# Optimization experiments

Measured on AMD Instinct MI355X. Metric: run time of the kernel, lower is better.

The kernel has to match this reference:

```python
import jax, jax.numpy as jnp
import numpy as np

NUM_HEAD = 8
HIDDEN = 128
NLAYERS = 6
NUM_FREQ = HIDDEN // 2


def make_pe_table(w):
    # relative positions in [-(w-1), w-1] -> raw angle table (the torch code
    # indexes `pe` BEFORE sin/cos are applied, so the table holds raw angles)
    rel = jnp.arange(w)[None, :] - jnp.arange(w)[:, None]          # [w, w]
    idx = (rel + (w - 1)).reshape(-1)
    rel_s2l = jnp.arange(2 * w - 1, dtype=jnp.float32) - (w - 1)   # [2w-1]
    freqs = jnp.arange(NUM_FREQ * 2)
    dim = jnp.power(jnp.float32(10000.0), (2 * (freqs // 2) / HIDDEN).astype(jnp.float32))
    pe = rel_s2l[:, None] / dim[None, :]                           # [2w-1, 128]
    return pe[idx].reshape(w, w, HIDDEN)


def layer_norm(x, g, b, eps=1e-5):
    mu = x.mean(-1, keepdims=True)
    var = ((x - mu) ** 2).mean(-1, keepdims=True)
    return (x - mu) / jnp.sqrt(var + eps) * g + b


def attention(Wi, bi, Wo, bo, query, key, pe_table, is_cross):
    w, h, c = query.shape
    hd = c // NUM_HEAD
    if is_cross:
        q = query @ Wi[:c].T + bi[:c]
        kv = key @ Wi[c:].T + bi[c:]
        k, v = jnp.split(kv, 2, axis=-1)
    else:
        q, k, v = jnp.split(query @ Wi.T + bi, 3, axis=-1)
    q = q.reshape(w, h, NUM_HEAD, hd)
    k = k.reshape(w, h, NUM_HEAD, hd)
    v = v.reshape(w, h, NUM_HEAD, hd)
    attn = jnp.einsum('whnc,vhnc->hnwv', q, k)                      # [h, nh, w, w]
    # relative PE terms: project pe_table with the q and k input projections
    rpe = pe_table @ Wi[:2 * c].T + bi[:2 * c]                       # [w, w, 2c]
    q_rpe, k_rpe = jnp.split(rpe, 2, axis=-1)
    q_rpe = q_rpe.reshape(w, w, NUM_HEAD, hd)
    k_rpe = k_rpe.reshape(w, w, NUM_HEAD, hd)
    attn = attn + jnp.einsum('wnec,wvec->newv', q, k_rpe) + jnp.einsum('vnec,wvec->newv', k, q_rpe)
    attn = attn / (hd ** 0.5)
    score = attn.sum(axis=1)                                         # [h, w, w]
    p = jax.nn.softmax(attn, axis=-1)
    out = jnp.einsum('hnwv,vhnc->whnc', p, v).reshape(w, h, c)
    return out @ Wo.T + bo, score


# mirror torch.utils.checkpoint on every attention call
_self_attn = jax.checkpoint(lambda Wi, bi, Wo, bo, x, pe: attention(Wi, bi, Wo, bo, x, x, pe, False))
_cross_attn = jax.checkpoint(lambda Wi, bi, Wo, bo, q, k, pe: attention(Wi, bi, Wo, bo, q, k, pe, True))


def forward(x_l, x_r, feat_w, feat_b, self_Wi, self_bi, self_Wo, self_bo,
            cross_Wi, cross_bi, cross_Wo, cross_bo, ln_g, ln_b):
    b, c, h, w = x_l.shape
    # FeatEx modeled as learned 1x1 conv c -> HIDDEN
    xl = jnp.einsum('bchw,dc->bdhw', x_l, feat_w) + feat_b[None, :, None, None]
    xr = jnp.einsum('bchw,dc->bdhw', x_r, feat_w) + feat_b[None, :, None, None]
    pe_table = make_pe_table(w)
    # (b,c,h,w) -> (w, h*b, c): width is the sequence axis
    xl = xl.transpose(3, 2, 0, 1).reshape(w, h * b, HIDDEN)
    xr = xr.transpose(3, 2, 0, 1).reshape(w, h * b, HIDDEN)
    cross_score = None
    for i in range(NLAYERS):
        xl = layer_norm(xl, ln_g, ln_b)
        o, _ = _self_attn(self_Wi[i], self_bi[i], self_Wo[i], self_bo[i], xl, pe_table)
        xl = xl + o
        xr = layer_norm(xr, ln_g, ln_b)
        o, _ = _self_attn(self_Wi[i], self_bi[i], self_Wo[i], self_bo[i], xr, pe_table)
        xr = xr + o
        xl = layer_norm(xl, ln_g, ln_b)
        xr = layer_norm(xr, ln_g, ln_b)
        o, cross_score = _cross_attn(cross_Wi[i], cross_bi[i], cross_Wo[i], cross_bo[i], xr, xl, pe_table)
        xl = xl + o
    u = jnp.arange(w, dtype=jnp.float32)
    corresp = (jax.nn.softmax(cross_score, axis=-1) * u[None, None, :]).sum(-1)  # [h*b, w]
    return u[None, None, :] - corresp.reshape(b, h, w)


def setup_inputs() -> dict:
    key = jax.random.key(0)
    ks = jax.random.split(key, 8)
    b, cin, h, w = 2, 128, 64, 224
    s = 0.02
    return {
        'x_l': jax.random.normal(ks[0], (b, cin, h, w), jnp.float32),
        'x_r': jax.random.normal(ks[1], (b, cin, h, w), jnp.float32),
        'feat_w': jax.random.normal(ks[2], (HIDDEN, cin), jnp.float32) * s,
        'feat_b': jnp.zeros((HIDDEN,), jnp.float32),
        'self_Wi': jax.random.normal(ks[3], (NLAYERS, 3 * HIDDEN, HIDDEN), jnp.float32) * s,
        'self_bi': jnp.zeros((NLAYERS, 3 * HIDDEN), jnp.float32),
        'self_Wo': jax.random.normal(ks[4], (NLAYERS, HIDDEN, HIDDEN), jnp.float32) * s,
        'self_bo': jnp.zeros((NLAYERS, HIDDEN), jnp.float32),
        'cross_Wi': jax.random.normal(ks[5], (NLAYERS, 3 * HIDDEN, HIDDEN), jnp.float32) * s,
        'cross_bi': jnp.zeros((NLAYERS, 3 * HIDDEN), jnp.float32),
        'cross_Wo': jax.random.normal(ks[6], (NLAYERS, HIDDEN, HIDDEN), jnp.float32) * s,
        'cross_bo': jnp.zeros((NLAYERS, HIDDEN), jnp.float32),
        'ln_g': jnp.ones((HIDDEN,), jnp.float32),
        'ln_b': jnp.zeros((HIDDEN,), jnp.float32),
    }


def reference(x_l, x_r, feat_w, feat_b, self_Wi, self_bi, self_Wo, self_bo,
              cross_Wi, cross_bi, cross_Wo, cross_bo, ln_g, ln_b):
    return forward(x_l, x_r, feat_w, feat_b, self_Wi, self_bi, self_Wo, self_bo,
                   cross_Wi, cross_bi, cross_Wo, cross_bo, ln_g, ln_b)
```

## Files before the change

### kernel.cpp

```cpp
#include <hip/hip_runtime.h>

typedef unsigned short u16;
typedef unsigned int u32;

#define W_ 224
#define H_ 128
#define C_ 128
#define NH 8
#define HD 16
#define ROWS_ (W_ * H_)
#define PREP_STRIDE 4128
#define KSTR 40
#define VSTR 232
#define TROWS 32

typedef __bf16 bf16x8 __attribute__((ext_vector_type(8)));
typedef float f32x4 __attribute__((ext_vector_type(4)));

__device__ __forceinline__ u16 f2bf(float f) {
  u32 u = __float_as_uint(f);
  return (u16)((u + 0x7FFFu + ((u >> 16) & 1u)) >> 16);
}
__device__ __forceinline__ u32 cvtpk(float lo, float hi) {
  u32 r;
  asm("v_cvt_pk_bf16_f32 %0, %1, %2" : "=v"(r) : "v"(lo), "v"(hi));
  return r;
}

__global__ __launch_bounds__(256) void prep_kernel(
    const float* __restrict__ self_Wi, const float* __restrict__ self_bi,
    const float* __restrict__ cross_Wi, const float* __restrict__ cross_bi,
    float* __restrict__ prep) {
  __shared__ float Wq[16][132];
  __shared__ float Wk[16][132];
  __shared__ float u[128];
  __shared__ float Aq[16], Ak[16], bq[16], bk[16];
  const int s = blockIdx.x, e = blockIdx.y, l = s >> 1;
  const float* Wi = (s & 1) ? cross_Wi + (size_t)l * 384 * 128 : self_Wi + (size_t)l * 384 * 128;
  const float* bi = (s & 1) ? cross_bi + l * 384 : self_bi + l * 384;
  const int tid = threadIdx.x;
  if (tid < 128) {
    float ex = (float)(tid & ~1) * (1.f / 128.f);
    u[tid] = expf(-ex * logf(10000.f));
  }
  if (tid >= 128 && tid < 144) { int r = tid - 128; bq[r] = bi[e * 16 + r]; }
  if (tid >= 160 && tid < 176) { int r = tid - 160; bk[r] = bi[128 + e * 16 + r]; }
  for (int t = tid; t < 2048; t += 256) {
    int r = t >> 7, f = t & 127;
    Wq[r][f] = Wi[(size_t)(e * 16 + r) * 128 + f];
    Wk[r][f] = Wi[(size_t)(128 + e * 16 + r) * 128 + f];
  }
  __syncthreads();
  {
    const int grp = tid >> 3;
    const int lg = tid & 7;
    const float* row = (grp < 16) ? Wq[grp] : Wk[grp - 16];
    float a = 0.f;
#pragma unroll
    for (int i = 0; i < 16; ++i) a += row[lg * 16 + i] * u[lg * 16 + i];
    a += __shfl_xor(a, 1);
    a += __shfl_xor(a, 2);
    a += __shfl_xor(a, 4);
    if (lg == 0) {
      if (grp < 16) Aq[grp] = a;
      else          Ak[grp - 16] = a;
    }
  }
  __syncthreads();
  float* out = prep + (size_t)s * PREP_STRIDE;
  for (int t = tid; t < 512; t += 256) {
    int v = t >> 7, f = t & 127;
    float acc = 0.f;
#pragma unroll
    for (int c = 0; c < 16; ++c) {
      if (v == 0)      acc += Wq[c][f] * Ak[c];
      else if (v == 1) acc += Wq[c][f] * bk[c];
      else if (v == 2) acc += Wk[c][f] * Aq[c];
      else             acc += Wk[c][f] * bq[c];
    }
    out[v * 1024 + e * 128 + f] = acc * 0.25f;
  }
  if (tid < 4) {
    int v = tid;
    float acc = 0.f;
#pragma unroll
    for (int c = 0; c < 16; ++c) {
      if (v == 0)      acc += bq[c] * Ak[c];
      else if (v == 1) acc += bq[c] * bk[c];
      else if (v == 2) acc += bk[c] * Aq[c];
      else             acc += bk[c] * bq[c];
    }
    out[4096 + v * 8 + e] = acc * 0.25f;
  }
}

__global__ __launch_bounds__(256) void tab_kernel(
    float* __restrict__ x, const float* __restrict__ g,
    const float* __restrict__ b, const float* __restrict__ wq,
    const float* __restrict__ cq, float* __restrict__ outA, float* __restrict__ outB,
    const float* __restrict__ wk, const float* __restrict__ ck,
    float* __restrict__ outG, float* __restrict__ outD,
    u16* __restrict__ xb, int mode) {
  __shared__ float ys[TROWS][132];
  __shared__ float ws[32][132];
  const int tid = threadIdx.x;
  for (int t = tid; t < 2048; t += 256) ws[t >> 7][t & 127] = wq[t];
  for (int t = tid; t < 2048; t += 256) ws[16 + (t >> 7)][t & 127] = wk[t];
  const int wv = tid >> 6, lane = tid & 63;
  const int base = blockIdx.x * TROWS;
  {
    float2 gg = ((const float2*)g)[lane];
    float2 bb = ((const float2*)b)[lane];
    for (int t = 0; t < TROWS / 4; ++t) {
      const int r = wv * (TROWS / 4) + t;
      float2* xp = (float2*)(x + (size_t)(base + r) * 128);
      float2 v = xp[lane];
      float s1 = v.x + v.y, s2 = v.x * v.x + v.y * v.y;
#pragma unroll
      for (int k = 1; k < 64; k <<= 1) {
        s1 += __shfl_xor(s1, k);
        s2 += __shfl_xor(s2, k);
      }
      float mean = s1 * (1.f / 128.f);
      float var = s2 * (1.f / 128.f) - mean * mean;
      float rstd = rsqrtf(var + 1e-5f);
      float y0 = (v.x - mean) * rstd * gg.x + bb.x;
      float y1 = (v.y - mean) * rstd * gg.y + bb.y;
      xp[lane] = make_float2(y0, y1);
      ((u32*)xb)[(size_t)(base + r) * 64 + lane] = cvtpk(y0, y1);
      ys[r][2 * lane] = y0;
      ys[r][2 * lane + 1] = y1;
    }
  }
  __syncthreads();
  const int c = tid & 31;
  const int rg = (tid >> 5) * 4;
  const int side = c >> 4, oo = c & 15;
  const float* wrow = ws[c];
  const int val = oo >> 3, e = oo & 7;
  const float cadd = side ? ck[val * 8 + e] : cq[val * 8 + e];
  float* dst = side ? (val ? outD : outG) : (val ? outB : outA);
#pragma unroll
  for (int rr = 0; rr < 4; ++rr) {
    const int p = base + rg + rr;
    const int half = (p >= ROWS_) ? 1 : 0;
    const int ploc = p - half * ROWS_;
    const bool active = (mode == 0) || (half ? (side == 0) : (side == 1));
    if (active) {
      const float* yr = ys[rg + rr];
      float a0 = 0.f, a1 = 0.f, a2 = 0.f, a3 = 0.f;
#pragma unroll 4
      for (int f = 0; f < 128; f += 4) {
        a0 += yr[f] * wrow[f];
        a1 += yr[f + 1] * wrow[f + 1];
        a2 += yr[f + 2] * wrow[f + 2];
        a3 += yr[f + 3] * wrow[f + 3];
      }
      float acc = (a0 + a1) + (a2 + a3);
      int i = ploc >> 7, blow = ploc & 127;
      int b_out = (mode == 0) ? half * 128 + blow : blow;
      dst[((size_t)(b_out * 8 + e)) * 224 + i] = acc + cadd;
    }
  }
}

__global__ __launch_bounds__(256) void gemm_plain(
    const u16* __restrict__ A, const u16* __restrict__ B,
    const float* __restrict__ bias, int mode, float* __restrict__ fout) {
  __shared__ u16 As[64 * 136];
  __shared__ u16 Bs[64 * 136];
  const int tid = threadIdx.x;
  const int M0 = blockIdx.x * 64, N0 = blockIdx.y * 64;
  const uint4* Ag = (const uint4*)(A + (size_t)M0 * 128);
  const uint4* Bg = (const uint4*)(B + (size_t)N0 * 128);
  for (int t = tid; t < 1024; t += 256) {
    int row = t >> 4, cc = t & 15;
    *(uint4*)&As[row * 136 + cc * 8] = Ag[row * 16 + cc];
  }
  for (int t = tid; t < 1024; t += 256) {
    int row = t >> 4, cc = t & 15;
    *(uint4*)&Bs[row * 136 + cc * 8] = Bg[row * 16 + cc];
  }
  __syncthreads();
  const int wave = tid >> 6, lane = tid & 63;
  const int wm = (wave >> 1) * 32, wn = (wave & 1) * 32;
  const int lr = lane & 15, kq = (lane >> 4) * 8;
  f32x4 acc[2][2] = {};
#pragma unroll
  for (int ks = 0; ks < 4; ++ks) {
    int ko = ks * 32 + kq;
    bf16x8 a0 = *(const bf16x8*)&As[(wm + lr) * 136 + ko];
    bf16x8 a1 = *(const bf16x8*)&As[(wm + 16 + lr) * 136 + ko];
    bf16x8 b0 = *(const bf16x8*)&Bs[(wn + lr) * 136 + ko];
    bf16x8 b1 = *(const bf16x8*)&Bs[(wn + 16 + lr) * 136 + ko];
    acc[0][0] = __builtin_amdgcn_mfma_f32_16x16x32_bf16(a0, b0, acc[0][0], 0, 0, 0);
    acc[0][1] = __builtin_amdgcn_mfma_f32_16x16x32_bf16(a0, b1, acc[0][1], 0, 0, 0);
    acc[1][0] = __builtin_amdgcn_mfma_f32_16x16x32_bf16(a1, b0, acc[1][0], 0, 0, 0);
    acc[1][1] = __builtin_amdgcn_mfma_f32_16x16x32_bf16(a1, b1, acc[1][1], 0, 0, 0);
  }
  const int colq = lane & 15, rowq = (lane >> 4) * 4;
#pragma unroll
  for (int tm = 0; tm < 2; ++tm)
#pragma unroll
    for (int tn = 0; tn < 2; ++tn) {
#pragma unroll
      for (int r = 0; r < 4; ++r) {
        int row = M0 + wm + tm * 16 + rowq + r;
        int col = N0 + wn + tn * 16 + colq;
        float v = acc[tm][tn][r] + bias[col];
        if (mode == 4) fout[(size_t)row * 128 + col] += v;
        else           fout[(size_t)row * 128 + col] = v;
      }
    }
}

__global__ __launch_bounds__(256) void gemm_qkv_self(
    const u16* __restrict__ X, const u16* __restrict__ Bw,
    const float* __restrict__ bias, u16* __restrict__ o0, u16* __restrict__ o1,
    u16* __restrict__ o2) {
  __shared__ u16 As[64 * 136];
  __shared__ u16 Bs[128 * 136];
  const int tid = threadIdx.x;
  const int M0 = blockIdx.x * 64, N0 = blockIdx.y * 128;
  {
    const uint4* Bg = (const uint4*)(Bw + (size_t)N0 * 128);
    for (int t = tid; t < 2048; t += 256) {
      int row = t >> 4, cc = t & 15;
      *(uint4*)&Bs[row * 136 + cc * 8] = Bg[row * 16 + cc];
    }
  }
  {
    const uint4* Ag = (const uint4*)(X + (size_t)M0 * 128);
    for (int t = tid; t < 1024; t += 256) {
      int row = t >> 4, cc = t & 15;
      *(uint4*)&As[row * 136 + cc * 8] = Ag[row * 16 + cc];
    }
  }
  __syncthreads();
  const int wave = tid >> 6, lane = tid & 63;
  const int wm = (wave >> 1) * 32, wn = (wave & 1) * 64;
  const int lr = lane & 15, kq = (lane >> 4) * 8;
  f32x4 acc[2][4] = {};
#pragma unroll
  for (int ks = 0; ks < 4; ++ks) {
    int ko = ks * 32 + kq;
    bf16x8 a0 = *(const bf16x8*)&As[(wm + lr) * 136 + ko];
    bf16x8 a1 = *(const bf16x8*)&As[(wm + 16 + lr) * 136 + ko];
#pragma unroll
    for (int tn = 0; tn < 4; ++tn) {
      bf16x8 b0 = *(const bf16x8*)&Bs[(wn + tn * 16 + lr) * 136 + ko];
      acc[0][tn] = __builtin_amdgcn_mfma_f32_16x16x32_bf16(a0, b0, acc[0][tn], 0, 0, 0);
      acc[1][tn] = __builtin_amdgcn_mfma_f32_16x16x32_bf16(a1, b0, acc[1][tn], 0, 0, 0);
    }
  }
  const int colq = lane & 15, rowq = (lane >> 4) * 4;
#pragma unroll
  for (int tm = 0; tm < 2; ++tm)
#pragma unroll
    for (int tn = 0; tn < 4; ++tn) {
#pragma unroll
      for (int r = 0; r < 4; ++r) {
        int row = M0 + wm + tm * 16 + rowq + r;
        int col = N0 + wn + tn * 16 + colq;
        float v = acc[tm][tn][r] + bias[col];
        int part = col >> 7;
        int cc = col & 127;
        int e = cc >> 4, c = cc & 15;
        int rloc = row, badd = 0;
        if (row >= ROWS_) { rloc = row - ROWS_; badd = 128; }
        int b = (rloc & 127) + badd, pos = rloc >> 7;
        size_t off = ((size_t)(b * NH + e) * W_ + pos) * HD + c;
        if (part == 0)      o0[off] = f2bf(v * 0.25f);
        else if (part == 1) o1[off] = f2bf(v);
        else                o2[off] = f2bf(v);
      }
    }
}

__global__ __launch_bounds__(256) void gemm_qkv_cross(
    const u16* __restrict__ Xl, const u16* __restrict__ Xr,
    const u16* __restrict__ cWi, const float* __restrict__ cbi,
    u16* __restrict__ QB, u16* __restrict__ KB, u16* __restrict__ VB) {
  __shared__ u16 As[64 * 136];
  __shared__ u16 Bs[128 * 136];
  const int tid = threadIdx.x;
  const int M0 = blockIdx.x * 64;
  const int y = blockIdx.y;
  const u16* X = (y == 0) ? Xr : Xl;
  const u16* Bw = cWi + (size_t)y * 128 * 128;
  const float* bias = cbi + y * 128;
  {
    const uint4* Bg = (const uint4*)Bw;
    for (int t = tid; t < 2048; t += 256) {
      int row = t >> 4, cc = t & 15;
      *(uint4*)&Bs[row * 136 + cc * 8] = Bg[row * 16 + cc];
    }
  }
  {
    const uint4* Ag = (const uint4*)(X + (size_t)M0 * 128);
    for (int t = tid; t < 1024; t += 256) {
      int row = t >> 4, cc = t & 15;
      *(uint4*)&As[row * 136 + cc * 8] = Ag[row * 16 + cc];
    }
  }
  __syncthreads();
  const int wave = tid >> 6, lane = tid & 63;
  const int wm = (wave >> 1) * 32, wn = (wave & 1) * 64;
  const int lr = lane & 15, kq = (lane >> 4) * 8;
  f32x4 acc[2][4] = {};
#pragma unroll
  for (int ks = 0; ks < 4; ++ks) {
    int ko = ks * 32 + kq;
    bf16x8 a0 = *(const bf16x8*)&As[(wm + lr) * 136 + ko];
    bf16x8 a1 = *(const bf16x8*)&As[(wm + 16 + lr) * 136 + ko];
#pragma unroll
    for (int tn = 0; tn < 4; ++tn) {
      bf16x8 b0 = *(const bf16x8*)&Bs[(wn + tn * 16 + lr) * 136 + ko];
      acc[0][tn] = __builtin_amdgcn_mfma_f32_16x16x32_bf16(a0, b0, acc[0][tn], 0, 0, 0);
      acc[1][tn] = __builtin_amdgcn_mfma_f32_16x16x32_bf16(a1, b0, acc[1][tn], 0, 0, 0);
    }
  }
  u16* outp = (y == 0) ? QB : ((y == 1) ? KB : VB);
  const float scale = (y == 0) ? 0.25f : 1.f;
  const int colq = lane & 15, rowq = (lane >> 4) * 4;
#pragma unroll
  for (int tm = 0; tm < 2; ++tm)
#pragma unroll
    for (int tn = 0; tn < 4; ++tn) {
#pragma unroll
      for (int r = 0; r < 4; ++r) {
        int row = M0 + wm + tm * 16 + rowq + r;
        int col = wn + tn * 16 + colq;
        float v = (acc[tm][tn][r] + bias[col]) * scale;
        int e = col >> 4, c = col & 15;
        int b = row & 127, pos = row >> 7;
        outp[((size_t)(b * NH + e) * W_ + pos) * HD + c] = f2bf(v);
      }
    }
}

__global__ __launch_bounds__(448) void attn_kernel(
    const u16* __restrict__ qb, const u16* __restrict__ kb,
    const u16* __restrict__ vb, const float* __restrict__ ALPHA,
    const float* __restrict__ BETA, const float* __restrict__ GAMMA,
    const float* __restrict__ DELTA, u16* __restrict__ obuf) {
  __shared__ u16 Ksh[224 * KSTR];
  __shared__ u16 Qsh[224 * KSTR];
  __shared__ u16 Vt[16 * VSTR];
  __shared__ u16 Pbuf[7][16 * KSTR];
  const int e = blockIdx.x, b = blockIdx.y;
  const size_t hb = (size_t)(b * NH + e);
  const int tid = threadIdx.x;
  const u32 ONE = 0x3F80u;

  if (tid < 224) {
    const int j = tid;
    const uint4* src = (const uint4*)(kb + (hb * W_ + j) * HD);
    uint4 a = src[0], b2 = src[1];
    *(uint4*)&Ksh[j * KSTR] = a;
    *(uint4*)&Ksh[j * KSTR + 8] = b2;
    float G = GAMMA[hb * 224 + j];
    float D = DELTA[hb * 224 + j];
    float jf = (float)j;
    float P = G * jf + D;
    u16 Phi = f2bf(P);
    float Plo = P - __uint_as_float((u32)Phi << 16);
    u32* ex = (u32*)&Ksh[j * KSTR + 16];
    ex[0] = (u32)f2bf(G) | ((u32)Phi << 16);
    ex[1] = (u32)f2bf(Plo) | ((u32)f2bf(jf) << 16);
    ex[2] = ONE | (ONE << 16);
#pragma unroll
    for (int z = 3; z < 12; ++z) ex[z] = 0;
    const uint4* vsrc = (const uint4*)(vb + (hb * W_ + j) * HD);
    uint4 va = vsrc[0], vb4 = vsrc[1];
    u32 w[8] = {va.x, va.y, va.z, va.w, vb4.x, vb4.y, vb4.z, vb4.w};
#pragma unroll
    for (int c = 0; c < 16; ++c)
      Vt[c * VSTR + j] = (c & 1) ? (u16)(w[c >> 1] >> 16) : (u16)(w[c >> 1] & 0xFFFF);
  } else {
    const int i = tid - 224;
    const uint4* src = (const uint4*)(qb + (hb * W_ + i) * HD);
    uint4 a = src[0], b2 = src[1];
    *(uint4*)&Qsh[i * KSTR] = a;
    *(uint4*)&Qsh[i * KSTR + 8] = b2;
    float al = ALPHA[hb * 224 + i];
    float be = BETA[hb * 224 + i];
    float ifl = (float)i;
    float Q = be - al * ifl;
    u16 Qhi = f2bf(Q);
    float Qlo = Q - __uint_as_float((u32)Qhi << 16);
    u32* ex = (u32*)&Qsh[i * KSTR + 16];
    ex[0] = (u32)f2bf(-ifl) | (ONE << 16);
    ex[1] = ONE | ((u32)f2bf(al) << 16);
    ex[2] = (u32)Qhi | ((u32)f2bf(Qlo) << 16);
#pragma unroll
    for (int z = 3; z < 12; ++z) ex[z] = 0;
  }
  __syncthreads();

  const int wid = tid >> 6, lane = tid & 63;
  const int g = lane >> 4, li = lane & 15;
  u16* pb = &Pbuf[wid][0];
  const int obase = (b & 128) ? ROWS_ : 0;
  const int blow = b & 127;

  for (int qt = wid * 2; qt < wid * 2 + 2; ++qt) {
    const int i0 = qt * 16;
    const bf16x8 Bq = *(const bf16x8*)&Qsh[(i0 + li) * KSTR + g * 8];
    f32x4 C[7][2];
#pragma unroll
    for (int js = 0; js < 7; ++js) {
      const bf16x8 A0 = *(const bf16x8*)&Ksh[(js * 32 + li) * KSTR + g * 8];
      const bf16x8 A1 = *(const bf16x8*)&Ksh[(js * 32 + 16 + li) * KSTR + g * 8];
      const f32x4 Z = {0.f, 0.f, 0.f, 0.f};
      C[js][0] = __builtin_amdgcn_mfma_f32_16x16x32_bf16(A0, Bq, Z, 0, 0, 0);
      C[js][1] = __builtin_amdgcn_mfma_f32_16x16x32_bf16(A1, Bq, Z, 0, 0, 0);
    }
    float m = -1e30f;
#pragma unroll
    for (int js = 0; js < 7; ++js)
#pragma unroll
      for (int h = 0; h < 2; ++h)
        m = fmaxf(m, fmaxf(fmaxf(C[js][h][0], C[js][h][1]), fmaxf(C[js][h][2], C[js][h][3])));
    m = fmaxf(m, __shfl_xor(m, 16));
    m = fmaxf(m, __shfl_xor(m, 32));
    f32x4 O = {0.f, 0.f, 0.f, 0.f};
    float lsum = 0.f;
#pragma unroll
    for (int js = 0; js < 7; ++js) {
      float p0 = __expf(C[js][0][0] - m), p1 = __expf(C[js][0][1] - m);
      float p2 = __expf(C[js][0][2] - m), p3 = __expf(C[js][0][3] - m);
      float p4 = __expf(C[js][1][0] - m), p5 = __expf(C[js][1][1] - m);
      float p6 = __expf(C[js][1][2] - m), p7 = __expf(C[js][1][3] - m);
      lsum += ((p0 + p1) + (p2 + p3)) + ((p4 + p5) + (p6 + p7));
      u16* pr = pb + li * KSTR + g * 4;
      *(uint2*)pr = make_uint2(cvtpk(p0, p1), cvtpk(p2, p3));
      *(uint2*)(pr + 16) = make_uint2(cvtpk(p4, p5), cvtpk(p6, p7));
      const bf16x8 Ap = *(const bf16x8*)&Pbuf[wid][li * KSTR + g * 8];
      const bf16x8 Bv = *(const bf16x8*)&Vt[li * VSTR + js * 32 + g * 8];
      O = __builtin_amdgcn_mfma_f32_16x16x32_bf16(Ap, Bv, O, 0, 0, 0);
    }
    lsum += __shfl_xor(lsum, 16);
    lsum += __shfl_xor(lsum, 32);
#pragma unroll
    for (int r = 0; r < 4; ++r) {
      const float lr = __shfl(lsum, g * 4 + r);
      const int irow = i0 + g * 4 + r;
      obuf[((size_t)(obase + irow * 128 + blow)) * C_ + e * HD + li] = f2bf(O[r] * (1.f / lr));
    }
  }
}

__global__ __launch_bounds__(256) void transpose_kernel(const float* __restrict__ x_l,
                                                        const float* __restrict__ x_r,
                                                        u16* __restrict__ xT) {
  __shared__ float tile[128][57];
  const int wt = blockIdx.x * 56, hi = blockIdx.y;
  const int img = blockIdx.z >> 1, bi = blockIdx.z & 1;
  const float* x = img ? x_r : x_l;
  const int wave = threadIdx.x >> 6, lane = threadIdx.x & 63;
  for (int c = wave; c < 128; c += 4) {
    if (lane < 56)
      tile[c][lane] = x[(((size_t)bi * 128 + c) * 64 + hi) * 224 + wt + lane];
  }
  __syncthreads();
  u32* dst = (u32*)xT;
  for (int w = wave; w < 56; w += 4) {
    int p = img * ROWS_ + (wt + w) * 128 + hi * 2 + bi;
    float a = tile[lane * 2][w], b2 = tile[lane * 2 + 1][w];
    dst[(size_t)p * 64 + lane] = (u32)f2bf(a) | ((u32)f2bf(b2) << 16);
  }
}

__global__ __launch_bounds__(448) void corresp_kernel(
    const u16* __restrict__ qb, const u16* __restrict__ kb,
    const float* __restrict__ ALPHA, const float* __restrict__ BETA,
    const float* __restrict__ GAMMA, const float* __restrict__ DELTA,
    float* __restrict__ out) {
  __shared__ u16 Ksh[224 * 136];
  __shared__ float Gs[224], Ds[224];
  const int b = blockIdx.x, tid = threadIdx.x;
  if (tid < 224) {
    const int j = tid;
#pragma unroll
    for (int e = 0; e < 8; ++e) {
      const uint4* src = (const uint4*)(kb + ((size_t)(b * 8 + e) * 224 + j) * 16);
      *(uint4*)&Ksh[j * 136 + e * 16] = src[0];
      *(uint4*)&Ksh[j * 136 + e * 16 + 8] = src[1];
    }
    float gs = 0.f, ds = 0.f;
#pragma unroll
    for (int e = 0; e < 8; ++e) {
      gs += GAMMA[((size_t)(b * 8 + e)) * 224 + j];
      ds += DELTA[((size_t)(b * 8 + e)) * 224 + j];
    }
    Gs[j] = gs;
    Ds[j] = ds;
  }
  __syncthreads();
  const int wid = tid >> 6, lane = tid & 63;
  const int g = lane >> 4, li = lane & 15;
  const int i = blockIdx.y * 112 + wid * 16 + li;
  bf16x8 Bq[4];
#pragma unroll
  for (int ks = 0; ks < 4; ++ks) {
    const int e2 = ks * 2 + (g >> 1), c0 = (g & 1) * 8;
    Bq[ks] = *(const bf16x8*)&qb[((size_t)(b * 8 + e2) * 224 + i) * 16 + c0];
  }
  f32x4 C[14];
#pragma unroll
  for (int js = 0; js < 14; ++js) {
    f32x4 acc = {0.f, 0.f, 0.f, 0.f};
#pragma unroll
    for (int ks = 0; ks < 4; ++ks) {
      const bf16x8 A = *(const bf16x8*)&Ksh[(js * 16 + li) * 136 + ks * 32 + g * 8];
      acc = __builtin_amdgcn_mfma_f32_16x16x32_bf16(A, Bq[ks], acc, 0, 0, 0);
    }
    C[js] = acc;
  }
  float ai = 0.f, bi_ = 0.f;
#pragma unroll
  for (int e = 0; e < 8; ++e) {
    ai += ALPHA[((size_t)(b * 8 + e)) * 224 + i];
    bi_ += BETA[((size_t)(b * 8 + e)) * 224 + i];
  }
  const float ifl = (float)i;
  float m = -1e30f;
#pragma unroll
  for (int js = 0; js < 14; ++js) {
#pragma unroll
    for (int r = 0; r < 4; ++r) {
      const int j = js * 16 + g * 4 + r;
      float s = C[js][r] + ((float)j - ifl) * (ai + Gs[j]) + bi_ + Ds[j];
      C[js][r] = s;
      m = fmaxf(m, s);
    }
  }
  m = fmaxf(m, __shfl_xor(m, 16));
  m = fmaxf(m, __shfl_xor(m, 32));
  float l = 0.f, wj = 0.f;
#pragma unroll
  for (int js = 0; js < 14; ++js) {
#pragma unroll
    for (int r = 0; r < 4; ++r) {
      const float p = __expf(C[js][r] - m);
      l += p;
      wj += p * (float)(js * 16 + g * 4 + r);
    }
  }
  l += __shfl_xor(l, 16);
  l += __shfl_xor(l, 32);
  wj += __shfl_xor(wj, 16);
  wj += __shfl_xor(wj, 32);
  if (g == 0) out[(size_t)b * 224 + i] = ifl - wj / fmaxf(l, 1e-30f);
}

#define OFF_FEAT 0
#define OFF_SWI 16384
#define OFF_SWO 311296
#define OFF_CWI 409600
#define OFF_CWO 704512
#define N_WALL 802816
__global__ __launch_bounds__(256) void cvt_all_kernel(
    const float* __restrict__ feat_w, const float* __restrict__ self_Wi,
    const float* __restrict__ self_Wo, const float* __restrict__ cross_Wi,
    const float* __restrict__ cross_Wo, u16* __restrict__ dst) {
  int idx = blockIdx.x * 256 + threadIdx.x;
  if (idx >= N_WALL) return;
  float v;
  if (idx < OFF_SWI)       v = feat_w[idx];
  else if (idx < OFF_SWO)  v = self_Wi[idx - OFF_SWI];
  else if (idx < OFF_CWI)  v = self_Wo[idx - OFF_SWO];
  else if (idx < OFF_CWO)  v = cross_Wi[idx - OFF_CWI];
  else                     v = cross_Wo[idx - OFF_CWO];
  dst[idx] = f2bf(v);
}

extern "C" void kernel_launch(void* const* d_in, const int* in_sizes, int n_in,
                              void* d_out, int out_size, void* d_ws, size_t ws_size,
                              hipStream_t stream) {
  (void)in_sizes; (void)n_in; (void)out_size; (void)ws_size;
  const float* x_l = (const float*)d_in[0];
  const float* x_r = (const float*)d_in[1];
  const float* feat_w = (const float*)d_in[2];
  const float* feat_b = (const float*)d_in[3];
  const float* self_Wi = (const float*)d_in[4];
  const float* self_bi = (const float*)d_in[5];
  const float* self_Wo = (const float*)d_in[6];
  const float* self_bo = (const float*)d_in[7];
  const float* cross_Wi = (const float*)d_in[8];
  const float* cross_bi = (const float*)d_in[9];
  const float* cross_Wo = (const float*)d_in[10];
  const float* cross_bo = (const float*)d_in[11];
  const float* ln_g = (const float*)d_in[12];
  const float* ln_b = (const float*)d_in[13];

  char* ws = (char*)d_ws;
  size_t off = 0;
  auto alloc = [&](size_t bytes) {
    char* p = ws + off;
    off += (bytes + 255) & ~(size_t)255;
    return p;
  };
  float* XA = (float*)alloc((size_t)2 * ROWS_ * C_ * 4);
  u16* QB = (u16*)alloc((size_t)256 * NH * W_ * HD * 2);
  u16* KB = (u16*)alloc((size_t)256 * NH * W_ * HD * 2);
  u16* VB = (u16*)alloc((size_t)256 * NH * W_ * HD * 2);
  u16* OB = (u16*)alloc((size_t)2 * ROWS_ * C_ * 2);
  u16* WALL = (u16*)alloc((size_t)N_WALL * 2);
  float* PREP = (float*)alloc((size_t)12 * PREP_STRIDE * 4);
  float* ALPHA = (float*)alloc((size_t)256 * NH * W_ * 4);
  float* BETA = (float*)alloc((size_t)256 * NH * W_ * 4);
  float* GAMMA = (float*)alloc((size_t)256 * NH * W_ * 4);
  float* DELTA = (float*)alloc((size_t)256 * NH * W_ * 4);
  u16* XB = OB;

  cvt_all_kernel<<<3136, 256, 0, stream>>>(feat_w, self_Wi, self_Wo, cross_Wi, cross_Wo, WALL);
  prep_kernel<<<dim3(12, 8), 256, 0, stream>>>(self_Wi, self_bi, cross_Wi, cross_bi, PREP);

  transpose_kernel<<<dim3(4, 64, 4), 256, 0, stream>>>(x_l, x_r, QB);
  gemm_plain<<<dim3(896, 2), 256, 0, stream>>>(QB, WALL + OFF_FEAT, feat_b, 5, XA);

  for (int l = 0; l < 6; ++l) {
    const u16* sWi = WALL + OFF_SWI + (size_t)l * 384 * 128;
    const u16* sWo = WALL + OFF_SWO + (size_t)l * 128 * 128;
    const u16* cWi = WALL + OFF_CWI + (size_t)l * 384 * 128;
    const u16* cWo = WALL + OFF_CWO + (size_t)l * 128 * 128;
    const float* sbi = self_bi + l * 384;
    const float* sbo = self_bo + l * 128;
    const float* cbi = cross_bi + l * 384;
    const float* cbo = cross_bo + l * 128;
    const float* ps = PREP + (size_t)(l * 2) * PREP_STRIDE;
    const float* pc = PREP + (size_t)(l * 2 + 1) * PREP_STRIDE;

    tab_kernel<<<1792, 256, 0, stream>>>(XA, ln_g, ln_b, ps, ps + 4096, ALPHA, BETA,
                                         ps + 2048, ps + 4112, GAMMA, DELTA, XB, 0);
    gemm_qkv_self<<<dim3(896, 3), 256, 0, stream>>>(XB, sWi, sbi, QB, KB, VB);
    attn_kernel<<<dim3(8, 256), 448, 0, stream>>>(QB, KB, VB, ALPHA, BETA, GAMMA, DELTA, OB);
    gemm_plain<<<dim3(896, 2), 256, 0, stream>>>(OB, sWo, sbo, 4, XA);

    tab_kernel<<<1792, 256, 0, stream>>>(XA, ln_g, ln_b, pc, pc + 4096, ALPHA, BETA,
                                         pc + 2048, pc + 4112, GAMMA, DELTA, XB, 1);
    gemm_qkv_cross<<<dim3(448, 3), 256, 0, stream>>>(XB, XB + (size_t)ROWS_ * C_, cWi, cbi,
                                                     QB, KB, VB);
    if (l < 5) {
      attn_kernel<<<dim3(8, 128), 448, 0, stream>>>(QB, KB, VB, ALPHA, BETA, GAMMA, DELTA, OB);
      gemm_plain<<<dim3(448, 2), 256, 0, stream>>>(OB, cWo, cbo, 4, XA);
    }
  }
  corresp_kernel<<<dim3(128, 2), 448, 0, stream>>>(QB, KB, ALPHA, BETA, GAMMA, DELTA,
                                                   (float*)d_out);
}
```

Baseline: 1.263 ms.

## Keep softmax probabilities in registers, use exp2, enlarge QKV GEMM tiles

```diff
diff --git a/kernel.cpp b/kernel.cpp
--- a/kernel.cpp
+++ b/kernel.cpp
@@ -26,6 +26,14 @@
   asm("v_cvt_pk_bf16_f32 %0, %1, %2" : "=v"(r) : "v"(lo), "v"(hi));
   return r;
 }
+__device__ __forceinline__ float bflo(u32 u) { return __uint_as_float(u << 16); }
+__device__ __forceinline__ float bfhi(u32 u) { return __uint_as_float(u & 0xFFFF0000u); }
+
+#if __has_builtin(__builtin_amdgcn_exp2f)
+#define EX2(x) __builtin_amdgcn_exp2f(x)
+#else
+#define EX2(x) __expf((x) * 0.6931471805599453f)
+#endif
 
 __global__ __launch_bounds__(256) void prep_kernel(
     const float* __restrict__ self_Wi, const float* __restrict__ self_bi,
@@ -102,7 +110,7 @@
     float* __restrict__ outG, float* __restrict__ outD,
     u16* __restrict__ xb, int mode) {
   __shared__ float ys[TROWS][132];
-  __shared__ float ws[32][132];
+  __shared__ float ws[32][133];
   const int tid = threadIdx.x;
   for (int t = tid; t < 2048; t += 256) ws[t >> 7][t & 127] = wq[t];
   for (int t = tid; t < 2048; t += 256) ws[16 + (t >> 7)][t & 127] = wk[t];
@@ -214,50 +222,45 @@
     }
 }
 
-__global__ __launch_bounds__(256) void gemm_qkv_self(
+__global__ __launch_bounds__(512) void gemm_qkv_self(
     const u16* __restrict__ X, const u16* __restrict__ Bw,
     const float* __restrict__ bias, u16* __restrict__ o0, u16* __restrict__ o1,
     u16* __restrict__ o2) {
-  __shared__ u16 As[64 * 136];
+  __shared__ u16 As[128 * 136];
   __shared__ u16 Bs[128 * 136];
   const int tid = threadIdx.x;
-  const int M0 = blockIdx.x * 64, N0 = blockIdx.y * 128;
+  const int M0 = blockIdx.x * 128, N0 = blockIdx.y * 128;
   {
     const uint4* Bg = (const uint4*)(Bw + (size_t)N0 * 128);
-    for (int t = tid; t < 2048; t += 256) {
-      int row = t >> 4, cc = t & 15;
-      *(uint4*)&Bs[row * 136 + cc * 8] = Bg[row * 16 + cc];
-    }
-  }
-  {
     const uint4* Ag = (const uint4*)(X + (size_t)M0 * 128);
-    for (int t = tid; t < 1024; t += 256) {
+    for (int t = tid; t < 2048; t += 512) {
       int row = t >> 4, cc = t & 15;
       *(uint4*)&As[row * 136 + cc * 8] = Ag[row * 16 + cc];
+      *(uint4*)&Bs[row * 136 + cc * 8] = Bg[row * 16 + cc];
     }
   }
   __syncthreads();
   const int wave = tid >> 6, lane = tid & 63;
-  const int wm = (wave >> 1) * 32, wn = (wave & 1) * 64;
+  const int wm = (wave >> 2) * 64, wn = (wave & 3) * 32;
   const int lr = lane & 15, kq = (lane >> 4) * 8;
-  f32x4 acc[2][4] = {};
+  f32x4 acc[4][2] = {};
 #pragma unroll
   for (int ks = 0; ks < 4; ++ks) {
     int ko = ks * 32 + kq;
-    bf16x8 a0 = *(const bf16x8*)&As[(wm + lr) * 136 + ko];
-    bf16x8 a1 = *(const bf16x8*)&As[(wm + 16 + lr) * 136 + ko];
-#pragma unroll
-    for (int tn = 0; tn < 4; ++tn) {
-      bf16x8 b0 = *(const bf16x8*)&Bs[(wn + tn * 16 + lr) * 136 + ko];
-      acc[0][tn] = __builtin_amdgcn_mfma_f32_16x16x32_bf16(a0, b0, acc[0][tn], 0, 0, 0);
-      acc[1][tn] = __builtin_amdgcn_mfma_f32_16x16x32_bf16(a1, b0, acc[1][tn], 0, 0, 0);
+    bf16x8 b0 = *(const bf16x8*)&Bs[(wn + lr) * 136 + ko];
+    bf16x8 b1 = *(const bf16x8*)&Bs[(wn + 16 + lr) * 136 + ko];
+#pragma unroll
+    for (int tm = 0; tm < 4; ++tm) {
+      bf16x8 a0 = *(const bf16x8*)&As[(wm + tm * 16 + lr) * 136 + ko];
+      acc[tm][0] = __builtin_amdgcn_mfma_f32_16x16x32_bf16(a0, b0, acc[tm][0], 0, 0, 0);
+      acc[tm][1] = __builtin_amdgcn_mfma_f32_16x16x32_bf16(a0, b1, acc[tm][1], 0, 0, 0);
     }
   }
   const int colq = lane & 15, rowq = (lane >> 4) * 4;
 #pragma unroll
-  for (int tm = 0; tm < 2; ++tm)
-#pragma unroll
-    for (int tn = 0; tn < 4; ++tn) {
+  for (int tm = 0; tm < 4; ++tm)
+#pragma unroll
+    for (int tn = 0; tn < 2; ++tn) {
 #pragma unroll
       for (int r = 0; r < 4; ++r) {
         int row = M0 + wm + tm * 16 + rowq + r;
@@ -277,56 +280,51 @@
     }
 }
 
-__global__ __launch_bounds__(256) void gemm_qkv_cross(
+__global__ __launch_bounds__(512) void gemm_qkv_cross(
     const u16* __restrict__ Xl, const u16* __restrict__ Xr,
     const u16* __restrict__ cWi, const float* __restrict__ cbi,
     u16* __restrict__ QB, u16* __restrict__ KB, u16* __restrict__ VB) {
-  __shared__ u16 As[64 * 136];
+  __shared__ u16 As[128 * 136];
   __shared__ u16 Bs[128 * 136];
   const int tid = threadIdx.x;
-  const int M0 = blockIdx.x * 64;
+  const int M0 = blockIdx.x * 128;
   const int y = blockIdx.y;
   const u16* X = (y == 0) ? Xr : Xl;
   const u16* Bw = cWi + (size_t)y * 128 * 128;
   const float* bias = cbi + y * 128;
   {
     const uint4* Bg = (const uint4*)Bw;
-    for (int t = tid; t < 2048; t += 256) {
-      int row = t >> 4, cc = t & 15;
-      *(uint4*)&Bs[row * 136 + cc * 8] = Bg[row * 16 + cc];
-    }
-  }
-  {
     const uint4* Ag = (const uint4*)(X + (size_t)M0 * 128);
-    for (int t = tid; t < 1024; t += 256) {
+    for (int t = tid; t < 2048; t += 512) {
       int row = t >> 4, cc = t & 15;
       *(uint4*)&As[row * 136 + cc * 8] = Ag[row * 16 + cc];
+      *(uint4*)&Bs[row * 136 + cc * 8] = Bg[row * 16 + cc];
     }
   }
   __syncthreads();
   const int wave = tid >> 6, lane = tid & 63;
-  const int wm = (wave >> 1) * 32, wn = (wave & 1) * 64;
+  const int wm = (wave >> 2) * 64, wn = (wave & 3) * 32;
   const int lr = lane & 15, kq = (lane >> 4) * 8;
-  f32x4 acc[2][4] = {};
+  f32x4 acc[4][2] = {};
 #pragma unroll
   for (int ks = 0; ks < 4; ++ks) {
     int ko = ks * 32 + kq;
-    bf16x8 a0 = *(const bf16x8*)&As[(wm + lr) * 136 + ko];
-    bf16x8 a1 = *(const bf16x8*)&As[(wm + 16 + lr) * 136 + ko];
-#pragma unroll
-    for (int tn = 0; tn < 4; ++tn) {
-      bf16x8 b0 = *(const bf16x8*)&Bs[(wn + tn * 16 + lr) * 136 + ko];
-      acc[0][tn] = __builtin_amdgcn_mfma_f32_16x16x32_bf16(a0, b0, acc[0][tn], 0, 0, 0);
-      acc[1][tn] = __builtin_amdgcn_mfma_f32_16x16x32_bf16(a1, b0, acc[1][tn], 0, 0, 0);
+    bf16x8 b0 = *(const bf16x8*)&Bs[(wn + lr) * 136 + ko];
+    bf16x8 b1 = *(const bf16x8*)&Bs[(wn + 16 + lr) * 136 + ko];
+#pragma unroll
+    for (int tm = 0; tm < 4; ++tm) {
+      bf16x8 a0 = *(const bf16x8*)&As[(wm + tm * 16 + lr) * 136 + ko];
+      acc[tm][0] = __builtin_amdgcn_mfma_f32_16x16x32_bf16(a0, b0, acc[tm][0], 0, 0, 0);
+      acc[tm][1] = __builtin_amdgcn_mfma_f32_16x16x32_bf16(a0, b1, acc[tm][1], 0, 0, 0);
     }
   }
   u16* outp = (y == 0) ? QB : ((y == 1) ? KB : VB);
   const float scale = (y == 0) ? 0.25f : 1.f;
   const int colq = lane & 15, rowq = (lane >> 4) * 4;
 #pragma unroll
-  for (int tm = 0; tm < 2; ++tm)
-#pragma unroll
-    for (int tn = 0; tn < 4; ++tn) {
+  for (int tm = 0; tm < 4; ++tm)
+#pragma unroll
+    for (int tn = 0; tn < 2; ++tn) {
 #pragma unroll
       for (int r = 0; r < 4; ++r) {
         int row = M0 + wm + tm * 16 + rowq + r;
@@ -347,11 +345,11 @@
   __shared__ u16 Ksh[224 * KSTR];
   __shared__ u16 Qsh[224 * KSTR];
   __shared__ u16 Vt[16 * VSTR];
-  __shared__ u16 Pbuf[7][16 * KSTR];
   const int e = blockIdx.x, b = blockIdx.y;
   const size_t hb = (size_t)(b * NH + e);
   const int tid = threadIdx.x;
   const u32 ONE = 0x3F80u;
+  const float LOG2E = 1.4426950408889634f;
 
   if (tid < 224) {
     const int j = tid;
@@ -362,11 +360,11 @@
     float G = GAMMA[hb * 224 + j];
     float D = DELTA[hb * 224 + j];
     float jf = (float)j;
-    float P = G * jf + D;
+    float P = (G * jf + D) * LOG2E;
     u16 Phi = f2bf(P);
     float Plo = P - __uint_as_float((u32)Phi << 16);
     u32* ex = (u32*)&Ksh[j * KSTR + 16];
-    ex[0] = (u32)f2bf(G) | ((u32)Phi << 16);
+    ex[0] = (u32)f2bf(G * LOG2E) | ((u32)Phi << 16);
     ex[1] = (u32)f2bf(Plo) | ((u32)f2bf(jf) << 16);
     ex[2] = ONE | (ONE << 16);
 #pragma unroll
@@ -374,24 +372,30 @@
     const uint4* vsrc = (const uint4*)(vb + (hb * W_ + j) * HD);
     uint4 va = vsrc[0], vb4 = vsrc[1];
     u32 w[8] = {va.x, va.y, va.z, va.w, vb4.x, vb4.y, vb4.z, vb4.w};
+    const int jl = j & 31;
+    const int qcol = (j & ~31) | (((jl >> 2) & 3) << 3) | ((jl >> 4) << 2) | (jl & 3);
 #pragma unroll
     for (int c = 0; c < 16; ++c)
-      Vt[c * VSTR + j] = (c & 1) ? (u16)(w[c >> 1] >> 16) : (u16)(w[c >> 1] & 0xFFFF);
+      Vt[c * VSTR + qcol] = (c & 1) ? (u16)(w[c >> 1] >> 16) : (u16)(w[c >> 1] & 0xFFFF);
   } else {
     const int i = tid - 224;
     const uint4* src = (const uint4*)(qb + (hb * W_ + i) * HD);
     uint4 a = src[0], b2 = src[1];
-    *(uint4*)&Qsh[i * KSTR] = a;
-    *(uint4*)&Qsh[i * KSTR + 8] = b2;
+    u32 qa[8] = {a.x, a.y, a.z, a.w, b2.x, b2.y, b2.z, b2.w};
+#pragma unroll
+    for (int t = 0; t < 8; ++t)
+      qa[t] = cvtpk(bflo(qa[t]) * LOG2E, bfhi(qa[t]) * LOG2E);
+    *(uint4*)&Qsh[i * KSTR] = make_uint4(qa[0], qa[1], qa[2], qa[3]);
+    *(uint4*)&Qsh[i * KSTR + 8] = make_uint4(qa[4], qa[5], qa[6], qa[7]);
     float al = ALPHA[hb * 224 + i];
     float be = BETA[hb * 224 + i];
     float ifl = (float)i;
-    float Q = be - al * ifl;
+    float Q = (be - al * ifl) * LOG2E;
     u16 Qhi = f2bf(Q);
     float Qlo = Q - __uint_as_float((u32)Qhi << 16);
     u32* ex = (u32*)&Qsh[i * KSTR + 16];
     ex[0] = (u32)f2bf(-ifl) | (ONE << 16);
-    ex[1] = ONE | ((u32)f2bf(al) << 16);
+    ex[1] = ONE | ((u32)f2bf(al * LOG2E) << 16);
     ex[2] = (u32)Qhi | ((u32)f2bf(Qlo) << 16);
 #pragma unroll
     for (int z = 3; z < 12; ++z) ex[z] = 0;
@@ -400,7 +404,6 @@
 
   const int wid = tid >> 6, lane = tid & 63;
   const int g = lane >> 4, li = lane & 15;
-  u16* pb = &Pbuf[wid][0];
   const int obase = (b & 128) ? ROWS_ : 0;
   const int blow = b & 127;
 
@@ -428,15 +431,13 @@
     float lsum = 0.f;
 #pragma unroll
     for (int js = 0; js < 7; ++js) {
-      float p0 = __expf(C[js][0][0] - m), p1 = __expf(C[js][0][1] - m);
-      float p2 = __expf(C[js][0][2] - m), p3 = __expf(C[js][0][3] - m);
-      float p4 = __expf(C[js][1][0] - m), p5 = __expf(C[js][1][1] - m);
-      float p6 = __expf(C[js][1][2] - m), p7 = __expf(C[js][1][3] - m);
+      float p0 = EX2(C[js][0][0] - m), p1 = EX2(C[js][0][1] - m);
+      float p2 = EX2(C[js][0][2] - m), p3 = EX2(C[js][0][3] - m);
+      float p4 = EX2(C[js][1][0] - m), p5 = EX2(C[js][1][1] - m);
+      float p6 = EX2(C[js][1][2] - m), p7 = EX2(C[js][1][3] - m);
       lsum += ((p0 + p1) + (p2 + p3)) + ((p4 + p5) + (p6 + p7));
-      u16* pr = pb + li * KSTR + g * 4;
-      *(uint2*)pr = make_uint2(cvtpk(p0, p1), cvtpk(p2, p3));
-      *(uint2*)(pr + 16) = make_uint2(cvtpk(p4, p5), cvtpk(p6, p7));
-      const bf16x8 Ap = *(const bf16x8*)&Pbuf[wid][li * KSTR + g * 8];
+      uint4 pu = make_uint4(cvtpk(p0, p1), cvtpk(p2, p3), cvtpk(p4, p5), cvtpk(p6, p7));
+      const bf16x8 Ap = __builtin_bit_cast(bf16x8, pu);
       const bf16x8 Bv = *(const bf16x8*)&Vt[li * VSTR + js * 32 + g * 8];
       O = __builtin_amdgcn_mfma_f32_16x16x32_bf16(Ap, Bv, O, 0, 0, 0);
     }
@@ -635,13 +636,13 @@
 
     tab_kernel<<<1792, 256, 0, stream>>>(XA, ln_g, ln_b, ps, ps + 4096, ALPHA, BETA,
                                          ps + 2048, ps + 4112, GAMMA, DELTA, XB, 0);
-    gemm_qkv_self<<<dim3(896, 3), 256, 0, stream>>>(XB, sWi, sbi, QB, KB, VB);
+    gemm_qkv_self<<<dim3(448, 3), 512, 0, stream>>>(XB, sWi, sbi, QB, KB, VB);
     attn_kernel<<<dim3(8, 256), 448, 0, stream>>>(QB, KB, VB, ALPHA, BETA, GAMMA, DELTA, OB);
     gemm_plain<<<dim3(896, 2), 256, 0, stream>>>(OB, sWo, sbo, 4, XA);
 
     tab_kernel<<<1792, 256, 0, stream>>>(XA, ln_g, ln_b, pc, pc + 4096, ALPHA, BETA,
                                          pc + 2048, pc + 4112, GAMMA, DELTA, XB, 1);
-    gemm_qkv_cross<<<dim3(448, 3), 256, 0, stream>>>(XB, XB + (size_t)ROWS_ * C_, cWi, cbi,
+    gemm_qkv_cross<<<dim3(224, 3), 512, 0, stream>>>(XB, XB + (size_t)ROWS_ * C_, cWi, cbi,
                                                      QB, KB, VB);
     if (l < 5) {
       attn_kernel<<<dim3(8, 128), 448, 0, stream>>>(QB, KB, VB, ALPHA, BETA, GAMMA, DELTA, OB);
```

After: 1.262 ms. About the same (-0.1%).
